# Kernel optimization log

Measured on AMD Instinct MI355X. Metric: run time of the kernel, lower is better.

## Reference

```python
import jax, jax.numpy as jnp
from jax import lax
import numpy as np

N_QUBITS = 8
Q_DEPTH = 10
DIM = 256  # 2**8

# basis-state bit table; wire 0 = most-significant bit (PennyLane convention)
_bits = ((np.arange(DIM)[:, None] >> (N_QUBITS - 1 - np.arange(N_QUBITS))) & 1)
# phase layer: S on even wires (phase i), T on odd wires (phase e^{i pi/4})
_ph = np.where(np.arange(N_QUBITS) % 2 == 0, 1j, np.exp(1j * np.pi / 4))
_diag = np.prod(np.power(_ph[None, :], _bits), axis=1)
# entangling_layer_3 CZ pattern
_cz = np.ones(DIM)
for i, j in [(0, 1), (2, 3), (4, 5), (6, 7), (1, 2), (3, 4), (5, 6)]:
    _cz = _cz * ((-1.0) ** (_bits[:, i] * _bits[:, j]))
DIAG = jnp.asarray((_diag * _cz).astype(np.complex64))  # phase+CZ layer fused diagonal
ZSIGNS = jnp.asarray((1 - 2 * _bits).astype(np.float32))  # [256, 8] PauliZ eigenvalues
H_GATE = jnp.asarray((np.array([[1.0, 1.0], [1.0, -1.0]]) / np.sqrt(2.0)).astype(np.complex64))
X_GATE = jnp.asarray(np.array([[0.0, 1.0], [1.0, 0.0]]).astype(np.complex64))
EYE2 = jnp.eye(2, dtype=jnp.complex64)
BN_EPS = 1e-5


def apply_1q(state, U, w):
    """Apply 2x2 gate U on wire w; state: [B, 2,2,...,2]."""
    state = jnp.moveaxis(state, w + 1, -1)
    state = jnp.matmul(state, U.T)
    return jnp.moveaxis(state, -1, w + 1)


def quantum_net(features, q_params):
    """Batched statevector sim of quantum_net_3. features [B,256], q_params [80] -> [B,8]."""
    f = features / jnp.linalg.norm(features, axis=1, keepdims=True)
    state = f.astype(jnp.complex64).reshape((-1,) + (2,) * N_QUBITS)
    for w in range(N_QUBITS):
        state = apply_1q(state, H_GATE, w)
    qw = q_params.reshape(Q_DEPTH, N_QUBITS)
    for layer in range(Q_DEPTH):
        for w in range(N_QUBITS):
            t = qw[layer, w]
            c = jnp.cos(t / 2).astype(jnp.complex64)
            s = jnp.sin(t / 2).astype(jnp.complex64)
            U = c * EYE2 + (-1j) * s * X_GATE  # RX(t)
            state = apply_1q(state, U, w)
        flat = state.reshape(-1, DIM) * DIAG  # phase layer + CZ entangling (diagonal)
        state = flat.reshape((-1,) + (2,) * N_QUBITS)
    sv = state.reshape(-1, DIM)
    probs = sv.real ** 2 + sv.imag ** 2
    return probs @ ZSIGNS  # [B, 8] expval(PauliZ_i)


def conv2d(x, w, b):
    y = lax.conv_general_dilated(x, w, (1, 1), 'SAME', dimension_numbers=('NCHW', 'OIHW', 'NCHW'))
    return y + b[None, :, None, None]


def bn(x, gamma, beta, mean, var):  # eval-mode BatchNorm2d
    inv = gamma / jnp.sqrt(var + BN_EPS)
    return x * inv[None, :, None, None] + (beta - mean * inv)[None, :, None, None]


def maxpool2(x):
    return lax.reduce_window(x, -jnp.inf, lax.max, (1, 1, 2, 2), (1, 1, 2, 2), 'VALID')


def setup_inputs() -> dict:
    key = jax.random.key(0)
    ks = jax.random.split(key, 16)
    B = 1024
    return {
        'x': jax.random.normal(ks[0], (B, 1, 28, 28), dtype=jnp.float32),
        'conv1_w': 0.1 * jax.random.normal(ks[1], (32, 1, 3, 3), dtype=jnp.float32),
        'conv1_b': jnp.zeros((32,), jnp.float32),
        'bn1_gamma': jnp.ones((32,), jnp.float32),
        'bn1_beta': jnp.zeros((32,), jnp.float32),
        'bn1_mean': jnp.zeros((32,), jnp.float32),
        'bn1_var': jnp.ones((32,), jnp.float32),
        'conv2_w': 0.05 * jax.random.normal(ks[2], (64, 32, 3, 3), dtype=jnp.float32),
        'conv2_b': jnp.zeros((64,), jnp.float32),
        'bn2_gamma': jnp.ones((64,), jnp.float32),
        'bn2_beta': jnp.zeros((64,), jnp.float32),
        'bn2_mean': jnp.zeros((64,), jnp.float32),
        'bn2_var': jnp.ones((64,), jnp.float32),
        'fc_w': 0.01 * jax.random.normal(ks[3], (256, 64 * 7 * 7), dtype=jnp.float32),
        'fc_b': jnp.zeros((256,), jnp.float32),
        'q_params': 0.1 * jax.random.normal(ks[4], (Q_DEPTH * N_QUBITS,), dtype=jnp.float32),
        'p1_w': 0.01 * jax.random.normal(ks[5], (128, 8), dtype=jnp.float32),
        'p1_b': jnp.zeros((128,), jnp.float32),
        'p2_w': 0.01 * jax.random.normal(ks[6], (64, 128), dtype=jnp.float32),
        'p2_b': jnp.zeros((64,), jnp.float32),
        'p3_w': 0.01 * jax.random.normal(ks[7], (10, 64), dtype=jnp.float32),
        'p3_b': jnp.zeros((10,), jnp.float32),
    }


def reference(x, conv1_w, conv1_b, bn1_gamma, bn1_beta, bn1_mean, bn1_var,
              conv2_w, conv2_b, bn2_gamma, bn2_beta, bn2_mean, bn2_var,
              fc_w, fc_b, q_params, p1_w, p1_b, p2_w, p2_b, p3_w, p3_b):
    h = maxpool2(jax.nn.relu(bn(conv2d(x, conv1_w, conv1_b), bn1_gamma, bn1_beta, bn1_mean, bn1_var)))
    h = maxpool2(jax.nn.relu(bn(conv2d(h, conv2_w, conv2_b), bn2_gamma, bn2_beta, bn2_mean, bn2_var)))
    h = h.reshape(h.shape[0], -1)  # [B, 64*7*7]
    feats = jnp.tanh(h @ fc_w.T + fc_b)  # [B, 256]
    q = quantum_net(feats, q_params)  # [B, 8]
    z = jax.nn.relu(q @ p1_w.T + p1_b)  # dropout = identity (eval)
    z = jax.nn.relu(z @ p2_w.T + p2_b)
    return z @ p3_w.T + p3_b
```

## Files before the change

kernel.cpp:

```cpp
#include <hip/hip_runtime.h>
#include <math.h>


#define B_SZ 1024

#define OFF_FCWP   0
#define OFF_W2F    802816
#define OFF_W1T    821248
#define OFF_SC1    821536
#define OFF_SH1    821568
#define OFF_SC2    821600
#define OFF_SH2    821664
#define OFF_H1     821728
#define OFF_H2P    7244256

#define KSPLIT_FC 14
#define KCHUNK_FC 224

typedef __attribute__((ext_vector_type(8))) short s16x8;
typedef __attribute__((ext_vector_type(4))) float f32x4;

__constant__ float C_COS8[8] = {1.f, 0.70710678f, 0.f, -0.70710678f, -1.f, -0.70710678f, 0.f, 0.70710678f};
__constant__ float C_SIN8[8] = {0.f, 0.70710678f, 1.f, 0.70710678f, 0.f, -0.70710678f, -1.f, -0.70710678f};

__device__ __forceinline__ unsigned short bf16_rne(float f) {
  unsigned u = __float_as_uint(f);
  unsigned r = u + 0x7FFFu + ((u >> 16) & 1u);
  return (unsigned short)(r >> 16);
}
__device__ __forceinline__ int div14(int m) {
  return __float2int_rz((float)m * 0.07142858f);
}
__device__ __forceinline__ int swz16(int e) {
  return e ^ (((e >> 6) & 3) << 3);
}

__global__ __launch_bounds__(256) void prep_kernel(
    const float* __restrict__ fc_w, const float* __restrict__ c2w, const float* __restrict__ c1w,
    const float* __restrict__ bn1g, const float* __restrict__ bn1b, const float* __restrict__ bn1m,
    const float* __restrict__ bn1v, const float* __restrict__ c1b,
    const float* __restrict__ bn2g, const float* __restrict__ bn2b, const float* __restrict__ bn2m,
    const float* __restrict__ bn2v, const float* __restrict__ c2b,
    float* __restrict__ ws) {
  int g = blockIdx.x * 256 + threadIdx.x;

  {
    int j = g & 7, lane = (g >> 3) & 63, nt = (g >> 9) & 15, kg = g >> 13;
    int n = nt * 16 + (lane & 15);
    int k = kg * 32 + ((lane >> 4) & 3) * 8 + j;
    float v = fc_w[n * 3136 + (k & 63) * 49 + (k >> 6)];
    unsigned short hi = bf16_rne(v);
    unsigned short lo = bf16_rne(v - __uint_as_float((unsigned)hi << 16));
    unsigned short* us = (unsigned short*)ws;
    int base = ((kg * 16 + nt) * 2) * 512 + lane * 8 + j;
    us[base] = hi;
    us[base + 512] = lo;
  }

  if (g < 36864) {
    int j = g & 7, L = (g >> 3) & 63, rest = g >> 9;
    int h = rest & 1; rest >>= 1;
    int t = rest % 9, w = rest / 9;
    int occ = w * 16 + (L & 15);
    int ic  = (L >> 4) * 8 + j;
    float v = c2w[occ * 288 + ic * 9 + t];
    unsigned short hi = bf16_rne(v);
    unsigned short res = hi;
    if (h) res = bf16_rne(v - __uint_as_float((unsigned)hi << 16));
    ((unsigned short*)(ws + OFF_W2F))[g] = res;
  }
  if (g < 288) {
    ws[OFF_W1T + g] = c1w[(g & 31) * 9 + (g >> 5)];
  }
  if (g < 32) {
    float inv = bn1g[g] / sqrtf(bn1v[g] + 1e-5f);
    ws[OFF_SC1 + g] = inv;
    ws[OFF_SH1 + g] = c1b[g] * inv + bn1b[g] - bn1m[g] * inv;
  }
  if (g < 64) {
    float inv = bn2g[g] / sqrtf(bn2v[g] + 1e-5f);
    ws[OFF_SC2 + g] = inv;
    ws[OFF_SH2 + g] = c2b[g] * inv + bn2b[g] - bn2m[g] * inv;
  }
}

__global__ __launch_bounds__(256, 2) void conv12_kernel(
    const float* __restrict__ x, const float* __restrict__ w1T,
    const float* __restrict__ sc1, const float* __restrict__ sh1,
    const float* __restrict__ w2f_f,
    const float* __restrict__ sc2, const float* __restrict__ sh2,
    unsigned short* __restrict__ h2hi, unsigned short* __restrict__ h2lo) {
  const int b = blockIdx.x, tid = threadIdx.x;
  const int lane = tid & 63, w = tid >> 6;

  __shared__ unsigned char lds_raw[50176];
  unsigned short* tile_hi = (unsigned short*)lds_raw;
  unsigned short* tile_lo = (unsigned short*)(lds_raw + 17408);
  float* xs  = (float*)(lds_raw + 34816);
  float* w1s = (float*)(lds_raw + 38656);
  float* sc1s = (float*)(lds_raw + 39808);
  float* sh1s = sc1s + 32;
  float* conv_out = (float*)lds_raw;

  {
    float4* z = (float4*)lds_raw;
    for (int i = tid; i < 2416; i += 256) z[i] = make_float4(0.f, 0.f, 0.f, 0.f);
  }
  __syncthreads();

  const float* xb = x + b * 784;
  for (int i = tid; i < 784; i += 256) {
    int y = i / 28, c = i - y * 28;
    xs[(y + 1) * 32 + (c + 1)] = xb[i];
  }
  for (int i = tid; i < 288; i += 256) w1s[i] = w1T[i];
  if (tid < 32) { sc1s[tid] = sc1[tid]; sh1s[tid] = sh1[tid]; }
  __syncthreads();

  for (int t = tid; t < 448; t += 256) {
    const int oc = t & 31, py = t >> 5;
    float wv[9];
#pragma unroll
    for (int k = 0; k < 9; ++k) wv[k] = w1s[k * 32 + oc];
    float acc0[28], acc1[28];
#pragma unroll
    for (int j = 0; j < 28; ++j) { acc0[j] = 0.f; acc1[j] = 0.f; }
#pragma unroll
    for (int r = 0; r < 4; ++r) {
      const int pr = 2 * py + r;
      float row[32];
#pragma unroll
      for (int q = 0; q < 8; ++q) {
        float4 v = *(const float4*)&xs[pr * 32 + 4 * q];
        row[4 * q] = v.x; row[4 * q + 1] = v.y; row[4 * q + 2] = v.z; row[4 * q + 3] = v.w;
      }
      if (r <= 2) {
#pragma unroll
        for (int kx = 0; kx < 3; ++kx) {
          const float w1v = wv[r * 3 + kx];
#pragma unroll
          for (int xx = 0; xx < 28; ++xx) acc0[xx] = fmaf(row[xx + kx], w1v, acc0[xx]);
        }
      }
      if (r >= 1) {
#pragma unroll
        for (int kx = 0; kx < 3; ++kx) {
          const float w1v = wv[(r - 1) * 3 + kx];
#pragma unroll
          for (int xx = 0; xx < 28; ++xx) acc1[xx] = fmaf(row[xx + kx], w1v, acc1[xx]);
        }
      }
    }
    const float sc = sc1s[oc], sh = sh1s[oc];
#pragma unroll
    for (int px = 0; px < 14; ++px) {
      float v0 = fmaxf(fmaf(acc0[2 * px], sc, sh), 0.f);
      float v1 = fmaxf(fmaf(acc0[2 * px + 1], sc, sh), 0.f);
      float v2 = fmaxf(fmaf(acc1[2 * px], sc, sh), 0.f);
      float v3 = fmaxf(fmaf(acc1[2 * px + 1], sc, sh), 0.f);
      float vm = fmaxf(fmaxf(v0, v1), fmaxf(v2, v3));
      unsigned short hv = bf16_rne(vm);
      unsigned short lv = bf16_rne(vm - __uint_as_float((unsigned)hv << 16));
      const int e = swz16(((py + 1) * 16 + (px + 1)) * 32 + oc);
      tile_hi[e] = hv;
      tile_lo[e] = lv;
    }
  }
  __syncthreads();

  const unsigned short* w2f = (const unsigned short*)w2f_f;
  s16x8 bf[9][2];
#pragma unroll
  for (int t = 0; t < 9; ++t)
#pragma unroll
    for (int h = 0; h < 2; ++h)
      bf[t][h] = *(const s16x8*)&w2f[(((w * 9 + t) * 2 + h) << 9) + lane * 8];

  f32x4 acc[13];
#pragma unroll
  for (int i = 0; i < 13; ++i) acc[i] = (f32x4){0.f, 0.f, 0.f, 0.f};

  const int kg8 = (lane >> 4) * 8;
#pragma unroll
  for (int mt = 0; mt < 13; ++mt) {
    const int m = mt * 16 + (lane & 15);
    const int y = div14(m), xx = m - y * 14;
    const int base = (y * 16 + xx) * 32 + kg8;
#pragma unroll
    for (int dy = 0; dy < 3; ++dy) {
#pragma unroll
      for (int dx = 0; dx < 3; ++dx) {
        const int off = swz16(base + (dy * 16 + dx) * 32);
        s16x8 ah = *(s16x8*)&tile_hi[off];
        s16x8 al = *(s16x8*)&tile_lo[off];
        const int t = dy * 3 + dx;
        acc[mt] = __builtin_amdgcn_mfma_f32_16x16x32_bf16(ah, bf[t][0], acc[mt], 0, 0, 0);
        acc[mt] = __builtin_amdgcn_mfma_f32_16x16x32_bf16(ah, bf[t][1], acc[mt], 0, 0, 0);
        acc[mt] = __builtin_amdgcn_mfma_f32_16x16x32_bf16(al, bf[t][0], acc[mt], 0, 0, 0);
      }
    }
  }
  __syncthreads();

  const int oc = w * 16 + (lane & 15);
  const float sc = sc2[oc], sh = sh2[oc];
  float* cw = conv_out + w * 3136;
#pragma unroll
  for (int mt = 0; mt < 13; ++mt) {
#pragma unroll
    for (int r = 0; r < 4; ++r) {
      const int m = mt * 16 + (lane >> 4) * 4 + r;
      if (m < 196) cw[m * 16 + (lane & 15)] = fmaxf(fmaf(acc[mt][r], sc, sh), 0.f);
    }
  }
  __syncthreads();

#pragma unroll
  for (int i = 0; i < 13; ++i) {
    const int ps = i * 4 + (lane >> 4);
    if (ps < 49) {
      const int py = (ps * 37) >> 8, px = ps - py * 7;
      const int m00 = py * 28 + px * 2;
      const int c0 = m00 * 16 + (lane & 15);
      float v0 = cw[c0], v1 = cw[c0 + 16], v2 = cw[c0 + 224], v3 = cw[c0 + 240];
      float vm = fmaxf(fmaxf(v0, v1), fmaxf(v2, v3));
      unsigned short hv = bf16_rne(vm);
      const int idx = b * 3136 + ps * 64 + oc;
      h2hi[idx] = hv;
      h2lo[idx] = bf16_rne(vm - __uint_as_float((unsigned)hv << 16));
    }
  }
}

__global__ __launch_bounds__(256) void fc_mfma_kernel(
    const unsigned short* __restrict__ h2hi, const unsigned short* __restrict__ h2lo,
    const unsigned short* __restrict__ Bfrag, float* __restrict__ Part) {
  __shared__ unsigned short Bs[8192];
  const int tid = threadIdx.x;
  const int lane = tid & 63, w = tid >> 6;
  const int m0 = blockIdx.y * 64, nt0 = blockIdx.x * 8, z = blockIdx.z;
  const int kz = z * KCHUNK_FC;

  const int mrow = m0 + w * 16 + (lane & 15);
  const int kg8 = (lane >> 4) * 8;
  const unsigned short* arow_hi = h2hi + mrow * 3136;
  const unsigned short* arow_lo = h2lo + mrow * 3136;

  f32x4 acc[8];
#pragma unroll
  for (int i = 0; i < 8; ++i) acc[i] = (f32x4){0.f, 0.f, 0.f, 0.f};

  for (int c = 0; c < 7; ++c) {
    const int kg = (kz >> 5) + c;
    {
      const uint4* src = (const uint4*)(Bfrag + (size_t)(kg * 16 + nt0) * 1024);
      uint4* dst = (uint4*)Bs;
#pragma unroll
      for (int i = 0; i < 4; ++i) dst[tid + 256 * i] = src[tid + 256 * i];
    }
    __syncthreads();

    const int k0 = kz + c * 32;
    s16x8 ah = *(const s16x8*)(arow_hi + k0 + kg8);
    s16x8 al = *(const s16x8*)(arow_lo + k0 + kg8);
#pragma unroll
    for (int nf = 0; nf < 8; ++nf) {
      s16x8 bh = *(s16x8*)&Bs[(nf * 2 + 0) * 512 + lane * 8];
      s16x8 bl = *(s16x8*)&Bs[(nf * 2 + 1) * 512 + lane * 8];
      acc[nf] = __builtin_amdgcn_mfma_f32_16x16x32_bf16(ah, bh, acc[nf], 0, 0, 0);
      acc[nf] = __builtin_amdgcn_mfma_f32_16x16x32_bf16(ah, bl, acc[nf], 0, 0, 0);
      acc[nf] = __builtin_amdgcn_mfma_f32_16x16x32_bf16(al, bh, acc[nf], 0, 0, 0);
    }
    __syncthreads();
  }

  float* dst = Part + (size_t)z * 262144;
  const int mbase = m0 + w * 16 + (lane >> 4) * 4;
  const int nbase = nt0 * 16 + (lane & 15);
#pragma unroll
  for (int nf = 0; nf < 8; ++nf) {
#pragma unroll
    for (int r = 0; r < 4; ++r) {
      dst[(mbase + r) * 256 + nbase + nf * 16] = acc[nf][r];
    }
  }
}

__global__ __launch_bounds__(256) void quantum_kernel(
    const float* __restrict__ Part, const float* __restrict__ fc_b,
    const float* __restrict__ qp,
    const float* __restrict__ p1w, const float* __restrict__ p1b,
    const float* __restrict__ p2w, const float* __restrict__ p2b,
    const float* __restrict__ p3w, const float* __restrict__ p3b,
    float* __restrict__ out) {
  const int b = blockIdx.x, tid = threadIdx.x;
  __shared__ float2 buf[2][256];
  __shared__ float csl[160];
  __shared__ float part[4][8];
  __shared__ float qv[8];
  __shared__ float z1[128];
  __shared__ float z2s[64];

  if (tid < 80) {
    float t = 0.5f * qp[tid];
    csl[2 * tid] = cosf(t);
    csl[2 * tid + 1] = sinf(t);
  }

  float f = fc_b[tid];
#pragma unroll
  for (int z = 0; z < KSPLIT_FC; ++z) f += Part[z * 262144 + b * 256 + tid];
  f = tanhf(f);

  float ss = f * f;
#pragma unroll
  for (int off = 32; off >= 1; off >>= 1) ss += __shfl_xor(ss, off);
  const int lane = tid & 63, wid = tid >> 6;
  if (lane == 0) part[wid][0] = ss;
  __syncthreads();
  const float tot = part[0][0] + part[1][0] + part[2][0] + part[3][0];
  const float inv = 1.0f / sqrtf(tot);
  float re = f * inv, im = 0.f;

  const int k8 = (2 * __popc(tid & 0xAA) + __popc(tid & 0x55)) & 7;
  float dre = C_COS8[k8], dim_ = C_SIN8[k8];
  {
    const int i = tid;
    int par = ((i >> 7) & (i >> 6)) ^ ((i >> 5) & (i >> 4)) ^ ((i >> 3) & (i >> 2)) ^ ((i >> 1) & i)
            ^ ((i >> 6) & (i >> 5)) ^ ((i >> 4) & (i >> 3)) ^ ((i >> 2) & (i >> 1));
    if (par & 1) { dre = -dre; dim_ = -dim_; }
  }

  int cur = 0;
  const float RS = 0.70710678118654752f;

#pragma unroll
  for (int w = 0; w < 2; ++w) {
    const int m = 128 >> w;
    cur ^= 1;
    buf[cur][tid] = make_float2(re, im);
    __syncthreads();
    float2 p = buf[cur][tid ^ m];
    float sgn = (tid & m) ? -1.f : 1.f;
    re = fmaf(sgn, re, p.x) * RS;
    im = fmaf(sgn, im, p.y) * RS;
  }
#pragma unroll
  for (int w = 2; w < 8; ++w) {
    const int m = 1 << (7 - w);
    float pre = __shfl_xor(re, m);
    float pim = __shfl_xor(im, m);
    float sgn = (tid & m) ? -1.f : 1.f;
    re = fmaf(sgn, re, pre) * RS;
    im = fmaf(sgn, im, pim) * RS;
  }

  for (int layer = 0; layer < 10; ++layer) {
    const float* cs = &csl[16 * layer];
#pragma unroll
    for (int w = 0; w < 2; ++w) {
      const int m = 128 >> w;
      const float c = cs[2 * w], s = cs[2 * w + 1];
      cur ^= 1;
      buf[cur][tid] = make_float2(re, im);
      __syncthreads();
      float2 p = buf[cur][tid ^ m];
      float nre = fmaf(s, p.y, c * re);
      float nim = fmaf(-s, p.x, c * im);
      re = nre; im = nim;
    }
#pragma unroll
    for (int w = 2; w < 8; ++w) {
      const int m = 1 << (7 - w);
      const float c = cs[2 * w], s = cs[2 * w + 1];
      float pre = __shfl_xor(re, m);
      float pim = __shfl_xor(im, m);
      float nre = fmaf(s, pim, c * re);
      float nim = fmaf(-s, pre, c * im);
      if (w == 7) {
        float tre = nre * dre - nim * dim_;
        nim = fmaf(nre, dim_, nim * dre);
        nre = tre;
      }
      re = nre; im = nim;
    }
  }

  const float prb = re * re + im * im;
#pragma unroll
  for (int w = 0; w < 8; ++w) {
    float v = ((tid >> (7 - w)) & 1) ? -prb : prb;
#pragma unroll
    for (int off = 32; off >= 1; off >>= 1) v += __shfl_xor(v, off);
    if (lane == 0) part[wid][w] = v;
  }
  __syncthreads();
  if (tid < 8) qv[tid] = part[0][tid] + part[1][tid] + part[2][tid] + part[3][tid];
  __syncthreads();

  if (tid < 128) {
    float a = p1b[tid];
#pragma unroll
    for (int k = 0; k < 8; ++k) a = fmaf(qv[k], p1w[tid * 8 + k], a);
    z1[tid] = fmaxf(a, 0.f);
  }
  __syncthreads();
  if (tid < 64) {
    float a = p2b[tid];
#pragma unroll 16
    for (int k = 0; k < 128; ++k) a = fmaf(z1[k], p2w[tid * 128 + k], a);
    z2s[tid] = fmaxf(a, 0.f);
  }
  __syncthreads();
  if (tid < 10) {
    float a = p3b[tid];
#pragma unroll 16
    for (int k = 0; k < 64; ++k) a = fmaf(z2s[k], p3w[tid * 64 + k], a);
    out[b * 10 + tid] = a;
  }
}

extern "C" void kernel_launch(void* const* d_in, const int* in_sizes, int n_in,
                              void* d_out, int out_size, void* d_ws, size_t ws_size,
                              hipStream_t stream) {
  (void)in_sizes; (void)n_in; (void)out_size; (void)ws_size;
  const float* x    = (const float*)d_in[0];
  const float* c1w  = (const float*)d_in[1];
  const float* c1b  = (const float*)d_in[2];
  const float* bn1g = (const float*)d_in[3];
  const float* bn1b = (const float*)d_in[4];
  const float* bn1m = (const float*)d_in[5];
  const float* bn1v = (const float*)d_in[6];
  const float* c2w  = (const float*)d_in[7];
  const float* c2b  = (const float*)d_in[8];
  const float* bn2g = (const float*)d_in[9];
  const float* bn2b = (const float*)d_in[10];
  const float* bn2m = (const float*)d_in[11];
  const float* bn2v = (const float*)d_in[12];
  const float* fc_w = (const float*)d_in[13];
  const float* fc_b = (const float*)d_in[14];
  const float* qp   = (const float*)d_in[15];
  const float* p1w  = (const float*)d_in[16];
  const float* p1b  = (const float*)d_in[17];
  const float* p2w  = (const float*)d_in[18];
  const float* p2b  = (const float*)d_in[19];
  const float* p3w  = (const float*)d_in[20];
  const float* p3b  = (const float*)d_in[21];
  float* ws = (float*)d_ws;
  float* outp = (float*)d_out;

  unsigned short* h2hi = (unsigned short*)(ws + OFF_H2P);
  unsigned short* h2lo = h2hi + 3211264;
  const unsigned short* bfrag = (const unsigned short*)ws;

  prep_kernel<<<3136, 256, 0, stream>>>(fc_w, c2w, c1w,
                                        bn1g, bn1b, bn1m, bn1v, c1b,
                                        bn2g, bn2b, bn2m, bn2v, c2b, ws);
  conv12_kernel<<<B_SZ, 256, 0, stream>>>(x, ws + OFF_W1T, ws + OFF_SC1, ws + OFF_SH1,
                                          ws + OFF_W2F, ws + OFF_SC2, ws + OFF_SH2,
                                          h2hi, h2lo);
  fc_mfma_kernel<<<dim3(2, 16, KSPLIT_FC), 256, 0, stream>>>(h2hi, h2lo, bfrag, ws + OFF_H1);
  quantum_kernel<<<B_SZ, 256, 0, stream>>>(ws + OFF_H1, fc_b, qp, p1w, p1b, p2w, p2b, p3w, p3b, outp);
}
```

Baseline: 166.6 us.

## Simulate each sample's quantum state in one wavefront with four amplitudes per lane

Rewrites the quantum kernel so a single 64-lane wavefront handles one sample's 256-amplitude statevector, with four amplitudes per lane. The two high wires become in-register butterflies, so the LDS exchanges and block-wide barriers per gate are gone, as are the cross-wave reductions. The grid drops to 256 blocks of four samples each. The post-quantum MLP now runs per wave, and p2w is transposed in the prep kernel so its reads are coalesced. In exchange, each thread uses more registers and the final dense layers have less parallelism per sample.

```diff
diff --git a/kernel.cpp b/kernel.cpp
--- a/kernel.cpp
+++ b/kernel.cpp
@@ -12,6 +12,7 @@
 #define OFF_SC2    821600
 #define OFF_SH2    821664
 #define OFF_H1     821728
+#define OFF_P2WT   4500000
 #define OFF_H2P    7244256
 
 #define KSPLIT_FC 14
@@ -41,6 +42,7 @@
     const float* __restrict__ bn1v, const float* __restrict__ c1b,
     const float* __restrict__ bn2g, const float* __restrict__ bn2b, const float* __restrict__ bn2m,
     const float* __restrict__ bn2v, const float* __restrict__ c2b,
+    const float* __restrict__ p2w,
     float* __restrict__ ws) {
   int g = blockIdx.x * 256 + threadIdx.x;
 
@@ -68,6 +70,9 @@
     unsigned short res = hi;
     if (h) res = bf16_rne(v - __uint_as_float((unsigned)hi << 16));
     ((unsigned short*)(ws + OFF_W2F))[g] = res;
+  }
+  if (g < 8192) {
+    ws[OFF_P2WT + g] = p2w[(g & 63) * 128 + (g >> 6)];
   }
   if (g < 288) {
     ws[OFF_W1T + g] = c1w[(g & 31) * 9 + (g >> 5)];
@@ -290,133 +295,173 @@
     const float* __restrict__ Part, const float* __restrict__ fc_b,
     const float* __restrict__ qp,
     const float* __restrict__ p1w, const float* __restrict__ p1b,
-    const float* __restrict__ p2w, const float* __restrict__ p2b,
+    const float* __restrict__ p2wT, const float* __restrict__ p2b,
     const float* __restrict__ p3w, const float* __restrict__ p3b,
     float* __restrict__ out) {
-  const int b = blockIdx.x, tid = threadIdx.x;
-  __shared__ float2 buf[2][256];
+  const int tid = threadIdx.x;
+  const int lane = tid & 63, wv = tid >> 6;
+  const int b = blockIdx.x * 4 + wv;
   __shared__ float csl[160];
-  __shared__ float part[4][8];
-  __shared__ float qv[8];
-  __shared__ float z1[128];
-  __shared__ float z2s[64];
+  __shared__ float z1buf[4][128];
+  __shared__ float z2buf[4][64];
 
   if (tid < 80) {
     float t = 0.5f * qp[tid];
     csl[2 * tid] = cosf(t);
     csl[2 * tid + 1] = sinf(t);
   }
-
-  float f = fc_b[tid];
-#pragma unroll
-  for (int z = 0; z < KSPLIT_FC; ++z) f += Part[z * 262144 + b * 256 + tid];
-  f = tanhf(f);
-
-  float ss = f * f;
+  __syncthreads();
+
+  float f[4];
+#pragma unroll
+  for (int r = 0; r < 4; ++r) {
+    const int n = r * 64 + lane;
+    float a = fc_b[n];
+#pragma unroll
+    for (int z = 0; z < KSPLIT_FC; ++z) a += Part[z * 262144 + b * 256 + n];
+    f[r] = tanhf(a);
+  }
+  float ss = (f[0] * f[0] + f[1] * f[1]) + (f[2] * f[2] + f[3] * f[3]);
 #pragma unroll
   for (int off = 32; off >= 1; off >>= 1) ss += __shfl_xor(ss, off);
-  const int lane = tid & 63, wid = tid >> 6;
-  if (lane == 0) part[wid][0] = ss;
-  __syncthreads();
-  const float tot = part[0][0] + part[1][0] + part[2][0] + part[3][0];
-  const float inv = 1.0f / sqrtf(tot);
-  float re = f * inv, im = 0.f;
-
-  const int k8 = (2 * __popc(tid & 0xAA) + __popc(tid & 0x55)) & 7;
-  float dre = C_COS8[k8], dim_ = C_SIN8[k8];
-  {
-    const int i = tid;
+  const float inv = 1.0f / sqrtf(ss);
+  float re[4], im[4];
+#pragma unroll
+  for (int r = 0; r < 4; ++r) { re[r] = f[r] * inv; im[r] = 0.f; }
+
+  float dre[4], dim_[4];
+#pragma unroll
+  for (int r = 0; r < 4; ++r) {
+    const int i = r * 64 + lane;
+    const int k8 = (2 * __popc(i & 0xAA) + __popc(i & 0x55)) & 7;
+    float dr = C_COS8[k8], di = C_SIN8[k8];
     int par = ((i >> 7) & (i >> 6)) ^ ((i >> 5) & (i >> 4)) ^ ((i >> 3) & (i >> 2)) ^ ((i >> 1) & i)
             ^ ((i >> 6) & (i >> 5)) ^ ((i >> 4) & (i >> 3)) ^ ((i >> 2) & (i >> 1));
-    if (par & 1) { dre = -dre; dim_ = -dim_; }
-  }
-
-  int cur = 0;
+    if (par & 1) { dr = -dr; di = -di; }
+    dre[r] = dr; dim_[r] = di;
+  }
+
   const float RS = 0.70710678118654752f;
 
-#pragma unroll
-  for (int w = 0; w < 2; ++w) {
-    const int m = 128 >> w;
-    cur ^= 1;
-    buf[cur][tid] = make_float2(re, im);
-    __syncthreads();
-    float2 p = buf[cur][tid ^ m];
-    float sgn = (tid & m) ? -1.f : 1.f;
-    re = fmaf(sgn, re, p.x) * RS;
-    im = fmaf(sgn, im, p.y) * RS;
+  {
+    float nr[4], ni[4];
+#pragma unroll
+    for (int r = 0; r < 4; ++r) {
+      const float sgn = (r & 2) ? -1.f : 1.f;
+      nr[r] = fmaf(sgn, re[r], re[r ^ 2]) * RS;
+      ni[r] = fmaf(sgn, im[r], im[r ^ 2]) * RS;
+    }
+#pragma unroll
+    for (int r = 0; r < 4; ++r) { re[r] = nr[r]; im[r] = ni[r]; }
+  }
+  {
+    float nr[4], ni[4];
+#pragma unroll
+    for (int r = 0; r < 4; ++r) {
+      const float sgn = (r & 1) ? -1.f : 1.f;
+      nr[r] = fmaf(sgn, re[r], re[r ^ 1]) * RS;
+      ni[r] = fmaf(sgn, im[r], im[r ^ 1]) * RS;
+    }
+#pragma unroll
+    for (int r = 0; r < 4; ++r) { re[r] = nr[r]; im[r] = ni[r]; }
   }
 #pragma unroll
   for (int w = 2; w < 8; ++w) {
     const int m = 1 << (7 - w);
-    float pre = __shfl_xor(re, m);
-    float pim = __shfl_xor(im, m);
-    float sgn = (tid & m) ? -1.f : 1.f;
-    re = fmaf(sgn, re, pre) * RS;
-    im = fmaf(sgn, im, pim) * RS;
+    const float sgn = (lane & m) ? -1.f : 1.f;
+#pragma unroll
+    for (int r = 0; r < 4; ++r) {
+      float pre = __shfl_xor(re[r], m);
+      float pim = __shfl_xor(im[r], m);
+      re[r] = fmaf(sgn, re[r], pre) * RS;
+      im[r] = fmaf(sgn, im[r], pim) * RS;
+    }
   }
 
   for (int layer = 0; layer < 10; ++layer) {
     const float* cs = &csl[16 * layer];
-#pragma unroll
-    for (int w = 0; w < 2; ++w) {
-      const int m = 128 >> w;
-      const float c = cs[2 * w], s = cs[2 * w + 1];
-      cur ^= 1;
-      buf[cur][tid] = make_float2(re, im);
-      __syncthreads();
-      float2 p = buf[cur][tid ^ m];
-      float nre = fmaf(s, p.y, c * re);
-      float nim = fmaf(-s, p.x, c * im);
-      re = nre; im = nim;
+    {
+      const float c = cs[0], s = cs[1];
+      float nr[4], ni[4];
+#pragma unroll
+      for (int r = 0; r < 4; ++r) {
+        nr[r] = fmaf(s, im[r ^ 2], c * re[r]);
+        ni[r] = fmaf(-s, re[r ^ 2], c * im[r]);
+      }
+#pragma unroll
+      for (int r = 0; r < 4; ++r) { re[r] = nr[r]; im[r] = ni[r]; }
+    }
+    {
+      const float c = cs[2], s = cs[3];
+      float nr[4], ni[4];
+#pragma unroll
+      for (int r = 0; r < 4; ++r) {
+        nr[r] = fmaf(s, im[r ^ 1], c * re[r]);
+        ni[r] = fmaf(-s, re[r ^ 1], c * im[r]);
+      }
+#pragma unroll
+      for (int r = 0; r < 4; ++r) { re[r] = nr[r]; im[r] = ni[r]; }
     }
 #pragma unroll
     for (int w = 2; w < 8; ++w) {
       const int m = 1 << (7 - w);
       const float c = cs[2 * w], s = cs[2 * w + 1];
-      float pre = __shfl_xor(re, m);
-      float pim = __shfl_xor(im, m);
-      float nre = fmaf(s, pim, c * re);
-      float nim = fmaf(-s, pre, c * im);
-      if (w == 7) {
-        float tre = nre * dre - nim * dim_;
-        nim = fmaf(nre, dim_, nim * dre);
-        nre = tre;
-      }
-      re = nre; im = nim;
-    }
-  }
-
-  const float prb = re * re + im * im;
+#pragma unroll
+      for (int r = 0; r < 4; ++r) {
+        float pre = __shfl_xor(re[r], m);
+        float pim = __shfl_xor(im[r], m);
+        float nre = fmaf(s, pim, c * re[r]);
+        float nim = fmaf(-s, pre, c * im[r]);
+        if (w == 7) {
+          float tre = nre * dre[r] - nim * dim_[r];
+          nim = fmaf(nre, dim_[r], nim * dre[r]);
+          nre = tre;
+        }
+        re[r] = nre; im[r] = nim;
+      }
+    }
+  }
+
+  float prb[4];
+#pragma unroll
+  for (int r = 0; r < 4; ++r) prb[r] = re[r] * re[r] + im[r] * im[r];
+  float qv[8];
 #pragma unroll
   for (int w = 0; w < 8; ++w) {
-    float v = ((tid >> (7 - w)) & 1) ? -prb : prb;
+    float v;
+    if (w == 0)      v = (prb[0] + prb[1]) - (prb[2] + prb[3]);
+    else if (w == 1) v = (prb[0] + prb[2]) - (prb[1] + prb[3]);
+    else {
+      const int m = 1 << (7 - w);
+      float s4 = (prb[0] + prb[1]) + (prb[2] + prb[3]);
+      v = (lane & m) ? -s4 : s4;
+    }
 #pragma unroll
     for (int off = 32; off >= 1; off >>= 1) v += __shfl_xor(v, off);
-    if (lane == 0) part[wid][w] = v;
-  }
-  __syncthreads();
-  if (tid < 8) qv[tid] = part[0][tid] + part[1][tid] + part[2][tid] + part[3][tid];
-  __syncthreads();
-
-  if (tid < 128) {
-    float a = p1b[tid];
-#pragma unroll
-    for (int k = 0; k < 8; ++k) a = fmaf(qv[k], p1w[tid * 8 + k], a);
-    z1[tid] = fmaxf(a, 0.f);
-  }
-  __syncthreads();
-  if (tid < 64) {
-    float a = p2b[tid];
+    qv[w] = v;
+  }
+
+  {
+    float a = p1b[lane], a2 = p1b[lane + 64];
+#pragma unroll
+    for (int k = 0; k < 8; ++k) {
+      a  = fmaf(qv[k], p1w[lane * 8 + k], a);
+      a2 = fmaf(qv[k], p1w[(lane + 64) * 8 + k], a2);
+    }
+    z1buf[wv][lane]      = fmaxf(a, 0.f);
+    z1buf[wv][lane + 64] = fmaxf(a2, 0.f);
+  }
+  float acc2 = p2b[lane];
 #pragma unroll 16
-    for (int k = 0; k < 128; ++k) a = fmaf(z1[k], p2w[tid * 128 + k], a);
-    z2s[tid] = fmaxf(a, 0.f);
-  }
-  __syncthreads();
-  if (tid < 10) {
-    float a = p3b[tid];
+  for (int k = 0; k < 128; ++k)
+    acc2 = fmaf(z1buf[wv][k], p2wT[k * 64 + lane], acc2);
+  z2buf[wv][lane] = fmaxf(acc2, 0.f);
+
+  if (lane < 10) {
+    float a3 = p3b[lane];
 #pragma unroll 16
-    for (int k = 0; k < 64; ++k) a = fmaf(z2s[k], p3w[tid * 64 + k], a);
-    out[b * 10 + tid] = a;
+    for (int k = 0; k < 64; ++k) a3 = fmaf(z2buf[wv][k], p3w[lane * 64 + k], a3);
+    out[b * 10 + lane] = a3;
   }
 }
 
@@ -455,10 +500,11 @@
 
   prep_kernel<<<3136, 256, 0, stream>>>(fc_w, c2w, c1w,
                                         bn1g, bn1b, bn1m, bn1v, c1b,
-                                        bn2g, bn2b, bn2m, bn2v, c2b, ws);
+                                        bn2g, bn2b, bn2m, bn2v, c2b, p2w, ws);
   conv12_kernel<<<B_SZ, 256, 0, stream>>>(x, ws + OFF_W1T, ws + OFF_SC1, ws + OFF_SH1,
                                           ws + OFF_W2F, ws + OFF_SC2, ws + OFF_SH2,
                                           h2hi, h2lo);
   fc_mfma_kernel<<<dim3(2, 16, KSPLIT_FC), 256, 0, stream>>>(h2hi, h2lo, bfrag, ws + OFF_H1);
-  quantum_kernel<<<B_SZ, 256, 0, stream>>>(ws + OFF_H1, fc_b, qp, p1w, p1b, p2w, p2b, p3w, p3b, outp);
-}
+  quantum_kernel<<<256, 256, 0, stream>>>(ws + OFF_H1, fc_b, qp, p1w, p1b,
+                                          ws + OFF_P2WT, p2b, p3w, p3b, outp);
+}
```

After: 165.8 us. About the same (-0.5%).
